# Performance work log

Measured on AMD Instinct MI355X. Metric: run time of the kernel, lower is better.

## Reference

```python
import jax, jax.numpy as jnp
import numpy as np

DEPTH = 8           # perfect binary tree depth -> 255 branches, 256 leaves
B = 524288          # number of input rows
F = 32              # number of features
N_OUT = 8           # outputs per leaf


def _build_tree(depth):
    """Replicates BaseTree.__init__'s enumerate_tree on a perfect binary tree.
    Returns cond, cond_mask of shape [n_leaf, n_branch] (bool)."""
    n_nodes = 2 ** (depth + 1) - 1
    n_branch = 2 ** depth - 1  # heap order: nodes < n_branch are branches
    is_branch = np.zeros(n_nodes, dtype=bool)
    node_conditions = np.zeros((n_nodes, n_nodes), dtype=bool)
    node_conditions_mask = np.zeros((n_nodes, n_nodes), dtype=bool)

    def enumerate_tree(node_id, parent_id=None):
        if parent_id is not None:
            node_conditions_mask[node_id] = node_conditions_mask[parent_id]
            node_conditions_mask[node_id][parent_id] = True
        if node_id < n_branch:
            left_id, right_id = 2 * node_id + 1, 2 * node_id + 2
            is_branch[node_id] = True
            node_conditions[left_id] = node_conditions[node_id]
            node_conditions[right_id] = node_conditions[node_id]
            node_conditions[right_id][node_id] = True
            enumerate_tree(left_id, node_id)
            enumerate_tree(right_id, node_id)

    enumerate_tree(0)
    is_leaf = ~is_branch
    branch_ids = np.nonzero(is_branch)[0]
    leaf_ids = np.nonzero(is_leaf)[0]
    cond = node_conditions[np.ix_(leaf_ids, branch_ids)]
    cond_mask = node_conditions_mask[np.ix_(leaf_ids, branch_ids)]
    return cond, cond_mask


def setup_inputs() -> dict:
    key = jax.random.key(0)
    k_x, k_t, k_v = jax.random.split(key, 3)
    cond_np, cond_mask_np = _build_tree(DEPTH)
    n_branch = cond_np.shape[1]
    rng = np.random.default_rng(0)
    feature = jnp.asarray(rng.integers(0, F, size=n_branch), dtype=jnp.int32)
    x = jax.random.normal(k_x, (B, F), dtype=jnp.float32)
    threshold = jax.random.normal(k_t, (n_branch,), dtype=jnp.float32) * 0.5
    value = jax.random.normal(k_v, (cond_np.shape[0], N_OUT), dtype=jnp.float32)
    return {
        "x": x,
        "feature": feature,
        "threshold": threshold,
        "cond": jnp.asarray(cond_np),            # [n_leaf, n_branch] bool
        "cond_mask": jnp.asarray(cond_mask_np),  # [n_leaf, n_branch] bool
        "value": value,                            # [n_leaf, n_out]
    }


def reference(x, feature, threshold, cond, cond_mask, value):
    # comparisons: [B, n_branch] int8 (x[:, feature] > threshold)
    comp = (x[:, feature] > threshold[None, :]).astype(jnp.int8)
    c8 = cond.astype(jnp.int8)
    m8 = cond_mask.astype(jnp.int8)
    # [B, n_leaf] int32 counts via int8 matmuls (accumulate in int32)
    cond_counts = jnp.matmul(comp, c8.T, preferred_element_type=jnp.int32)
    mask_counts = jnp.matmul(comp, m8.T, preferred_element_type=jnp.int32)
    cond_sum = jnp.sum(c8.astype(jnp.int32), axis=1)  # [n_leaf]
    no_false_neg = cond_counts == cond_sum[None, :]
    no_false_pos = cond_counts == mask_counts
    leaf_idx = jnp.argmax((no_false_neg & no_false_pos).astype(jnp.int32), axis=-1)
    return value[leaf_idx]  # [B, n_out]
```

## Files before the change

### kernel.cpp

```cpp
#include <hip/hip_runtime.h>

#define NB 255
#define DEPTH 8
#define F 32
#define XSTRIDE 36
#define ROWS_PER_WAVE 64
#define CHUNKS 2
#define WAVES 4
#define N_ROWS 524288

__global__ __launch_bounds__(256) void tree_traverse_pipelined(
    const float* __restrict__ x,
    const int*   __restrict__ feature,
    const float* __restrict__ threshold,
    const float* __restrict__ value,
    float*       __restrict__ out)
{
    __shared__ float xs[WAVES][ROWS_PER_WAVE * XSTRIDE];
    __shared__ int2  s_node[256];

    const int tid  = threadIdx.x;
    const int lane = tid & 63;
    const int wid  = tid >> 6;

    #pragma unroll
    for (int k = 0; k < 4; ++k) {
        int e = lane + 64 * k;
        if (e < NB) s_node[e] = make_int2(feature[e], __float_as_int(threshold[e]));
    }

    const int       gwave = blockIdx.x * WAVES + wid;
    const long long row0  = (long long)gwave * (ROWS_PER_WAVE * CHUNKS);
    const float4*   xg    = reinterpret_cast<const float4*>(x + row0 * F);

    float4 A[8], B[8];
    #pragma unroll
    for (int j = 0; j < 8; ++j) A[j] = xg[j * 64 + lane];
    #pragma unroll
    for (int j = 0; j < 8; ++j) B[j] = xg[512 + j * 64 + lane];

    float* myxs = xs[wid];
    const float* row_x = &myxs[lane * XSTRIDE];

    #pragma unroll
    for (int c = 0; c < CHUNKS; ++c) {
        #pragma unroll
        for (int j = 0; j < 8; ++j) {
            float4 v = (c == 0) ? A[j] : B[j];
            int f4idx = j * 64 + lane;
            int row   = f4idx >> 3;
            int cc    = f4idx & 7;
            *reinterpret_cast<float4*>(&myxs[row * XSTRIDE + cc * 4]) = v;
        }

        int node = 0;
        #pragma unroll
        for (int d = 0; d < DEPTH; ++d) {
            int2  nd = s_node[node];
            float t  = __int_as_float(nd.y);
            node = 2 * node + 1 + (row_x[nd.x] > t ? 1 : 0);
        }
        const int leaf = node - NB;

        const float4* v4 = reinterpret_cast<const float4*>(value + (size_t)leaf * 8);
        float4 v0 = v4[0];
        float4 v1 = v4[1];
        float4* o = reinterpret_cast<float4*>(out + (row0 + c * ROWS_PER_WAVE + lane) * 8);
        o[0] = v0;
        o[1] = v1;
    }
}

extern "C" void kernel_launch(void* const* d_in, const int* in_sizes, int n_in,
                              void* d_out, int out_size, void* d_ws, size_t ws_size,
                              hipStream_t stream) {
    (void)in_sizes; (void)n_in; (void)d_ws; (void)ws_size; (void)out_size;
    const float* x         = (const float*)d_in[0];
    const int*   feature   = (const int*)d_in[1];
    const float* threshold = (const float*)d_in[2];
    const float* value     = (const float*)d_in[5];
    float*       out       = (float*)d_out;

    dim3 grid(N_ROWS / (ROWS_PER_WAVE * CHUNKS * WAVES));
    dim3 block(256);
    tree_traverse_pipelined<<<grid, block, 0, stream>>>(x, feature, threshold, value, out);
}
```

Measured before the change: 19.47 us.

## Select features from per-thread registers instead of shared-memory transpose

Each thread now loads its full 32-feature row directly into registers and picks the split feature with a branch-free select tree, removing the LDS staging buffer and its writes and reads. Blocks now process 256 rows with one row per thread instead of two chunks per wave. This trades coalesced lane-contiguous global loads for strided per-thread row loads and adds roughly 250 select instructions per row.

```diff
diff --git a/kernel.cpp b/kernel.cpp
--- a/kernel.cpp
+++ b/kernel.cpp
@@ -3,72 +3,66 @@
 #define NB 255
 #define DEPTH 8
 #define F 32
-#define XSTRIDE 36
-#define ROWS_PER_WAVE 64
-#define CHUNKS 2
-#define WAVES 4
 #define N_ROWS 524288
 
-__global__ __launch_bounds__(256) void tree_traverse_pipelined(
+__device__ __forceinline__ float sel32(const float* v, int f) {
+    float a[16];
+#pragma unroll
+    for (int i = 0; i < 16; ++i) a[i] = (f & 1) ? v[2 * i + 1] : v[2 * i];
+    float b[8];
+#pragma unroll
+    for (int i = 0; i < 8; ++i) b[i] = (f & 2) ? a[2 * i + 1] : a[2 * i];
+    float c[4];
+#pragma unroll
+    for (int i = 0; i < 4; ++i) c[i] = (f & 4) ? b[2 * i + 1] : b[2 * i];
+    float d0 = (f & 8) ? c[1] : c[0];
+    float d1 = (f & 8) ? c[3] : c[2];
+    return (f & 16) ? d1 : d0;
+}
+
+__global__ __launch_bounds__(256) void tree_regsel_kernel(
     const float* __restrict__ x,
     const int*   __restrict__ feature,
     const float* __restrict__ threshold,
     const float* __restrict__ value,
     float*       __restrict__ out)
 {
-    __shared__ float xs[WAVES][ROWS_PER_WAVE * XSTRIDE];
-    __shared__ int2  s_node[256];
+    __shared__ int2 s_node[256];
 
     const int tid  = threadIdx.x;
     const int lane = tid & 63;
-    const int wid  = tid >> 6;
 
-    #pragma unroll
+#pragma unroll
     for (int k = 0; k < 4; ++k) {
         int e = lane + 64 * k;
         if (e < NB) s_node[e] = make_int2(feature[e], __float_as_int(threshold[e]));
     }
 
-    const int       gwave = blockIdx.x * WAVES + wid;
-    const long long row0  = (long long)gwave * (ROWS_PER_WAVE * CHUNKS);
-    const float4*   xg    = reinterpret_cast<const float4*>(x + row0 * F);
+    const long long row = (long long)blockIdx.x * 256 + tid;
+    const float4* xg = reinterpret_cast<const float4*>(x + row * F);
+    float v[32];
+#pragma unroll
+    for (int j = 0; j < 8; ++j) {
+        float4 t = xg[j];
+        v[4 * j + 0] = t.x; v[4 * j + 1] = t.y;
+        v[4 * j + 2] = t.z; v[4 * j + 3] = t.w;
+    }
 
-    float4 A[8], B[8];
-    #pragma unroll
-    for (int j = 0; j < 8; ++j) A[j] = xg[j * 64 + lane];
-    #pragma unroll
-    for (int j = 0; j < 8; ++j) B[j] = xg[512 + j * 64 + lane];
+    int node = 0;
+#pragma unroll
+    for (int d = 0; d < DEPTH; ++d) {
+        int2  nd = s_node[node];
+        float t  = __int_as_float(nd.y);
+        node = 2 * node + 1 + (sel32(v, nd.x) > t ? 1 : 0);
+    }
+    const int leaf = node - NB;
 
-    float* myxs = xs[wid];
-    const float* row_x = &myxs[lane * XSTRIDE];
-
-    #pragma unroll
-    for (int c = 0; c < CHUNKS; ++c) {
-        #pragma unroll
-        for (int j = 0; j < 8; ++j) {
-            float4 v = (c == 0) ? A[j] : B[j];
-            int f4idx = j * 64 + lane;
-            int row   = f4idx >> 3;
-            int cc    = f4idx & 7;
-            *reinterpret_cast<float4*>(&myxs[row * XSTRIDE + cc * 4]) = v;
-        }
-
-        int node = 0;
-        #pragma unroll
-        for (int d = 0; d < DEPTH; ++d) {
-            int2  nd = s_node[node];
-            float t  = __int_as_float(nd.y);
-            node = 2 * node + 1 + (row_x[nd.x] > t ? 1 : 0);
-        }
-        const int leaf = node - NB;
-
-        const float4* v4 = reinterpret_cast<const float4*>(value + (size_t)leaf * 8);
-        float4 v0 = v4[0];
-        float4 v1 = v4[1];
-        float4* o = reinterpret_cast<float4*>(out + (row0 + c * ROWS_PER_WAVE + lane) * 8);
-        o[0] = v0;
-        o[1] = v1;
-    }
+    const float4* v4 = reinterpret_cast<const float4*>(value + (size_t)leaf * 8);
+    float4 o0 = v4[0];
+    float4 o1 = v4[1];
+    float4* o = reinterpret_cast<float4*>(out + row * 8);
+    o[0] = o0;
+    o[1] = o1;
 }
 
 extern "C" void kernel_launch(void* const* d_in, const int* in_sizes, int n_in,
@@ -81,7 +75,7 @@
     const float* value     = (const float*)d_in[5];
     float*       out       = (float*)d_out;
 
-    dim3 grid(N_ROWS / (ROWS_PER_WAVE * CHUNKS * WAVES));
+    dim3 grid(N_ROWS / 256);
     dim3 block(256);
-    tree_traverse_pipelined<<<grid, block, 0, stream>>>(x, feature, threshold, value, out);
+    tree_regsel_kernel<<<grid, block, 0, stream>>>(x, feature, threshold, value, out);
 }
```

Result: slower. 74.69 us (+283.5%).
